# Optimization experiments

Measured on AMD Instinct MI355X. Metric: run time of the kernel, lower is better.

The kernel has to match this reference:

```python
import jax, jax.numpy as jnp
import numpy as np

COMMITMENT_COST = 0.25


def setup_inputs() -> dict:
    key = jax.random.key(0)
    k1, k2 = jax.random.split(key)
    x = jax.random.normal(k1, (32, 64, 64, 64), dtype=jnp.float32)  # NCHW, C=embedding_dim
    # nn.Embedding weight init: uniform(-1/num_embeddings, 1/num_embeddings)
    codebook = jax.random.uniform(k2, (512, 64), dtype=jnp.float32,
                                  minval=-1.0 / 512.0, maxval=1.0 / 512.0)
    return {"x": x, "codebook": codebook}


def reference(x, codebook):
    # NCHW -> NHWC
    inputs = jnp.transpose(x, (0, 2, 3, 1))  # [B,H,W,D]
    B, H, W, D = inputs.shape
    flat = inputs.reshape(-1, D)  # [N,D]
    # Squared Euclidean distances (argmin identical to torch.cdist's sqrt'ed distances)
    d2 = (jnp.sum(flat * flat, axis=1, keepdims=True)
          - 2.0 * flat @ codebook.T
          + jnp.sum(codebook * codebook, axis=1)[None, :])  # [N,K]
    idx = jnp.argmin(d2, axis=1)  # [N]
    quantized = codebook[idx].reshape(B, H, W, D)
    e_latent_loss = jnp.mean((jax.lax.stop_gradient(quantized) - inputs) ** 2)
    q_latent_loss = jnp.mean((quantized - jax.lax.stop_gradient(inputs)) ** 2)
    c_loss = q_latent_loss + COMMITMENT_COST * e_latent_loss
    # Straight-through estimator
    quantized = inputs + jax.lax.stop_gradient(quantized - inputs)
    quantized = jnp.transpose(quantized, (0, 3, 1, 2))  # NHWC -> NCHW
    return c_loss, quantized
```

## Files before the change

### kernel.cpp

```cpp
#include <hip/hip_runtime.h>
#include <hip/hip_bf16.h>


typedef __attribute__((ext_vector_type(8))) __bf16 bf16x8;
typedef __attribute__((ext_vector_type(4))) float f32x4;

#define WS_CBF   0
#define WS_HN2   65536
#define WS_RED   67584

#define K_XA   0
#define K_HN   8192
#define K_IDX  17408
#define K_RED  17664
#define K_SZ   17680

__device__ __forceinline__ unsigned f2b1(float f) {
  unsigned u = __float_as_uint(f);
  return (u + 0x7FFFu + ((u >> 16) & 1)) >> 16;
}
__device__ __forceinline__ unsigned pack2(float lo, float hi) {
  return f2b1(lo) | (f2b1(hi) << 16);
}
#if defined(__has_builtin)
#  if __has_builtin(__builtin_amdgcn_perm)
#    define PACKTR(lo, hi) __builtin_amdgcn_perm(__float_as_uint(hi), \
                             __float_as_uint(lo), 0x07060302u)
#  endif
#endif
#ifndef PACKTR
#  define PACKTR(lo, hi) ((__float_as_uint(hi) & 0xFFFF0000u) | \
                          (__float_as_uint(lo) >> 16))
#endif
__device__ __forceinline__ int swz(int row) {
  return ((row & 7) ^ ((row >> 4) & 7)) << 4;
}

__global__ void vq_prep(const float* __restrict__ cb, char* __restrict__ ws) {
  const int n = blockIdx.x * 64 + threadIdx.x;
  const float4* cb4 = (const float4*)cb;
  float4 f[16];
  #pragma unroll
  for (int j = 0; j < 16; ++j) f[j] = cb4[(n << 4) + j];
  float s = 0.f;
  #pragma unroll
  for (int j = 0; j < 16; ++j)
    s += f[j].x * f[j].x + f[j].y * f[j].y + f[j].z * f[j].z + f[j].w * f[j].w;
  ((float*)(ws + WS_HN2))[n] = 1.0f - 0.5f * s;
  const int ct = n >> 4, col = n & 15;
  #pragma unroll
  for (int kk = 0; kk < 2; ++kk) {
    #pragma unroll
    for (int g = 0; g < 4; ++g) {
      float4 a = f[kk * 8 + g * 2], b = f[kk * 8 + g * 2 + 1];
      uint4 u = {pack2(a.x, a.y), pack2(a.z, a.w), pack2(b.x, b.y), pack2(b.z, b.w)};
      *(uint4*)(ws + WS_CBF + (((ct << 1) + kk) << 10) + (((g << 4) | col) << 4)) = u;
    }
  }
}

__global__ void __launch_bounds__(128, 4)
vq_main(const float* __restrict__ x, const float* __restrict__ cb,
        const char* __restrict__ wsr, float* __restrict__ out,
        float* __restrict__ wsw) {
  __shared__ __align__(16) char smem[K_SZ];
  char*  xaz  = smem + K_XA;
  float* hn2z = (float*)(smem + K_HN);
  int*   idxz = (int*)(smem + K_IDX);
  float* redz = (float*)(smem + K_RED);
  float* qld2 = (float*)smem;

  const int t    = threadIdx.x;
  const int bid  = blockIdx.x;
  const int bimg = bid >> 6;
  const int hw0  = (bid & 63) << 6;
  const float4*  xb4 = (const float4*)(x + (bimg << 18) + hw0);
  const float4*  cb4 = (const float4*)cb;
  const bf16x8*  cbb = (const bf16x8*)(wsr + WS_CBF);

  float xsq = 0.f;
  {
    const int p  = t >> 2;
    const int r0 = (t & 3) << 4;
    #pragma unroll
    for (int j = 0; j < 4; ++j) {
      float4 A0 = xb4[((2 * p) << 10) + (r0 >> 2) + j];
      float4 A1 = xb4[((2 * p + 1) << 10) + (r0 >> 2) + j];
      const float* a0 = (const float*)&A0;
      const float* a1 = (const float*)&A1;
      #pragma unroll
      for (int u = 0; u < 4; ++u) {
        xsq = fmaf(a0[u], a0[u], xsq);
        xsq = fmaf(a1[u], a1[u], xsq);
        int r = r0 + (j << 2) + u;
        *(unsigned*)(xaz + r * 128 + ((p << 2) ^ swz(r))) = PACKTR(a0[u], a1[u]);
      }
    }
  }
  #pragma unroll
  for (int i = 0; i < 4; ++i)
    hn2z[t + (i << 7)] = ((const float*)(wsr + WS_HN2))[t + (i << 7)];
  __syncthreads();

  const int lane = t & 63;
  const int wid  = t >> 6;
  const int lrow = lane & 15;
  const int lk2  = (lane >> 4) << 4;

  bf16x8 af[2][2];
  #pragma unroll
  for (int s = 0; s < 2; ++s) {
    int row = (wid << 5) + (s << 4) + lrow;
    int sw = swz(row);
    af[s][0] = *(const bf16x8*)(xaz + row * 128 + (lk2 ^ sw));
    af[s][1] = *(const bf16x8*)(xaz + row * 128 + ((lk2 ^ 64) ^ sw));
  }

  unsigned bestu[2][4];
  #pragma unroll
  for (int s = 0; s < 2; ++s)
    #pragma unroll
    for (int r = 0; r < 4; ++r) bestu[s][r] = 0u;

  const unsigned tag0 = 511u - (unsigned)lrow;

  #pragma unroll 2
  for (int ct = 0; ct < 32; ++ct) {
    const bf16x8 b0 = cbb[(ct << 7) + lane];
    const bf16x8 b1 = cbb[(ct << 7) + 64 + lane];
    const float hv = hn2z[(ct << 4) + lrow];
    const unsigned tag = tag0 - (unsigned)(ct << 4);
    #pragma unroll
    for (int s = 0; s < 2; ++s) {
      f32x4 acc = {hv, hv, hv, hv};
      acc = __builtin_amdgcn_mfma_f32_16x16x32_bf16(af[s][0], b0, acc, 0, 0, 0);
      acc = __builtin_amdgcn_mfma_f32_16x16x32_bf16(af[s][1], b1, acc, 0, 0, 0);
      #pragma unroll
      for (int r = 0; r < 4; ++r) {
        unsigned key = (__float_as_uint(acc[r]) & 0xFFFFFE00u) | tag;
        bestu[s][r] = max(bestu[s][r], key);
      }
    }
  }

  float vsum = 0.f;
  #pragma unroll
  for (int s = 0; s < 2; ++s) {
    #pragma unroll
    for (int r = 0; r < 4; ++r) {
      unsigned k = bestu[s][r];
      #pragma unroll
      for (int m = 1; m <= 8; m <<= 1) {
        unsigned pk = __shfl_xor(k, m, 64);
        k = max(k, pk);
      }
      if (lrow == 0) {
        idxz[(wid << 5) + (s << 4) + ((lane >> 4) << 2) + r] =
            (int)(511u - (k & 511u));
        vsum += __uint_as_float(k & 0xFFFFFE00u) - 1.0f;
      }
    }
  }
  float lacc = xsq - 2.0f * vsum;
  #pragma unroll
  for (int m = 32; m; m >>= 1) lacc += __shfl_xor(lacc, m, 64);
  if (lane == 0) redz[wid] = lacc;
  __syncthreads();
  if (t == 0) wsw[bid] = redz[0] + redz[1];

  {
    const int myrow = t >> 1;
    const int chh   = t & 1;
    const int myidx = idxz[myrow];
    const float4* cbr = cb4 + (myidx << 4) + (chh << 3);
    #pragma unroll
    for (int j = 0; j < 8; ++j) {
      float4 v = cbr[j];
      const int d = (chh << 5) + (j << 2);
      qld2[(d + 0) * 68 + myrow] = v.x;
      qld2[(d + 1) * 68 + myrow] = v.y;
      qld2[(d + 2) * 68 + myrow] = v.z;
      qld2[(d + 3) * 68 + myrow] = v.w;
    }
  }
  __syncthreads();
  {
    float* outq = out + 1 + (bimg << 18) + hw0;
    const int r4 = (t & 15) << 2;
    const int d0 = t >> 4;
    #pragma unroll
    for (int i = 0; i < 8; ++i) {
      const int d = d0 + (i << 3);
      float4 v = *(const float4*)(qld2 + d * 68 + r4);
      *(float4*)(outq + (d << 12) + r4) = v;
    }
  }
}

__global__ void vq_finalize(const float* __restrict__ ws, float* __restrict__ out) {
  int t = threadIdx.x;
  __shared__ float red[4];
  float v = 0.f;
  #pragma unroll
  for (int k = 0; k < 8; ++k) v += ws[t + (k << 8)];
  #pragma unroll
  for (int m = 32; m; m >>= 1) v += __shfl_xor(v, m, 64);
  if ((t & 63) == 0) red[t >> 6] = v;
  __syncthreads();
  if (t == 0) out[0] = (red[0] + red[1] + red[2] + red[3]) * (1.25f / 8388608.0f);
}

extern "C" void kernel_launch(void* const* d_in, const int* in_sizes, int n_in,
                              void* d_out, int out_size, void* d_ws, size_t ws_size,
                              hipStream_t stream) {
  const float* x  = (const float*)d_in[0];
  const float* cb = (const float*)d_in[1];
  float* out = (float*)d_out;
  char*  ws  = (char*)d_ws;
  vq_prep<<<8, 64, 0, stream>>>(cb, ws);
  vq_main<<<2048, 128, 0, stream>>>(x, cb, ws, out, (float*)(ws + WS_RED));
  vq_finalize<<<1, 256, 0, stream>>>((float*)(ws + WS_RED), out);
}
```

Baseline: 33.94 us.

## Make each wavefront independent with private LDS regions and drop block barriers

Each of the two waves in a block now loads, transposes and gathers its own 32 rows in a private LDS region, which removes all three __syncthreads. The codebook-norm table is read straight from global (L1/L2-cached) memory instead of being staged into LDS. Per-wave partial losses are written out, so finalize sums twice as many entries. Nontemporal loads and stores are used for the streaming x input and the quantized output. The global norm reads inside the hot loop may add latency in exchange for less LDS traffic and no barriers.

```diff
diff --git a/kernel.cpp b/kernel.cpp
--- a/kernel.cpp
+++ b/kernel.cpp
@@ -9,11 +9,9 @@
 #define WS_HN2   65536
 #define WS_RED   67584
 
-#define K_XA   0
-#define K_HN   8192
-#define K_IDX  17408
-#define K_RED  17664
-#define K_SZ   17680
+#define WREG   9216
+#define K_IDX  18432
+#define K_SZ   18688
 
 __device__ __forceinline__ unsigned f2b1(float f) {
   unsigned u = __float_as_uint(f);
@@ -64,28 +62,30 @@
         const char* __restrict__ wsr, float* __restrict__ out,
         float* __restrict__ wsw) {
   __shared__ __align__(16) char smem[K_SZ];
-  char*  xaz  = smem + K_XA;
-  float* hn2z = (float*)(smem + K_HN);
-  int*   idxz = (int*)(smem + K_IDX);
-  float* redz = (float*)(smem + K_RED);
-  float* qld2 = (float*)smem;
-
   const int t    = threadIdx.x;
+  const int lane = t & 63;
+  const int wid  = t >> 6;
   const int bid  = blockIdx.x;
   const int bimg = bid >> 6;
-  const int hw0  = (bid & 63) << 6;
-  const float4*  xb4 = (const float4*)(x + (bimg << 18) + hw0);
-  const float4*  cb4 = (const float4*)cb;
-  const bf16x8*  cbb = (const bf16x8*)(wsr + WS_CBF);
+  const int wrow0 = ((bid & 63) << 6) + (wid << 5);
+
+  char*  xw   = smem + wid * WREG;
+  float* ovl  = (float*)(smem + wid * WREG);
+  int*   idxw = (int*)(smem + K_IDX) + (wid << 5);
+
+  const f32x4*  xb4  = (const f32x4*)(x + (bimg << 18) + wrow0);
+  const float4* cb4  = (const float4*)cb;
+  const bf16x8* cbb  = (const bf16x8*)(wsr + WS_CBF);
+  const float*  hn2g = (const float*)(wsr + WS_HN2);
 
   float xsq = 0.f;
   {
-    const int p  = t >> 2;
-    const int r0 = (t & 3) << 4;
+    const int p  = lane >> 1;
+    const int r0 = (lane & 1) << 4;
     #pragma unroll
     for (int j = 0; j < 4; ++j) {
-      float4 A0 = xb4[((2 * p) << 10) + (r0 >> 2) + j];
-      float4 A1 = xb4[((2 * p + 1) << 10) + (r0 >> 2) + j];
+      f32x4 A0 = __builtin_nontemporal_load(&xb4[((2 * p) << 10) + (r0 >> 2) + j]);
+      f32x4 A1 = __builtin_nontemporal_load(&xb4[((2 * p + 1) << 10) + (r0 >> 2) + j]);
       const float* a0 = (const float*)&A0;
       const float* a1 = (const float*)&A1;
       #pragma unroll
@@ -93,27 +93,21 @@
         xsq = fmaf(a0[u], a0[u], xsq);
         xsq = fmaf(a1[u], a1[u], xsq);
         int r = r0 + (j << 2) + u;
-        *(unsigned*)(xaz + r * 128 + ((p << 2) ^ swz(r))) = PACKTR(a0[u], a1[u]);
+        *(unsigned*)(xw + r * 128 + ((p << 2) ^ swz(r))) = PACKTR(a0[u], a1[u]);
       }
     }
   }
-  #pragma unroll
-  for (int i = 0; i < 4; ++i)
-    hn2z[t + (i << 7)] = ((const float*)(wsr + WS_HN2))[t + (i << 7)];
-  __syncthreads();
-
-  const int lane = t & 63;
-  const int wid  = t >> 6;
+
   const int lrow = lane & 15;
   const int lk2  = (lane >> 4) << 4;
 
   bf16x8 af[2][2];
   #pragma unroll
   for (int s = 0; s < 2; ++s) {
-    int row = (wid << 5) + (s << 4) + lrow;
+    int row = (s << 4) + lrow;
     int sw = swz(row);
-    af[s][0] = *(const bf16x8*)(xaz + row * 128 + (lk2 ^ sw));
-    af[s][1] = *(const bf16x8*)(xaz + row * 128 + ((lk2 ^ 64) ^ sw));
+    af[s][0] = *(const bf16x8*)(xw + row * 128 + (lk2 ^ sw));
+    af[s][1] = *(const bf16x8*)(xw + row * 128 + ((lk2 ^ 64) ^ sw));
   }
 
   unsigned bestu[2][4];
@@ -128,7 +122,7 @@
   for (int ct = 0; ct < 32; ++ct) {
     const bf16x8 b0 = cbb[(ct << 7) + lane];
     const bf16x8 b1 = cbb[(ct << 7) + 64 + lane];
-    const float hv = hn2z[(ct << 4) + lrow];
+    const float hv = hn2g[(ct << 4) + lrow];
     const unsigned tag = tag0 - (unsigned)(ct << 4);
     #pragma unroll
     for (int s = 0; s < 2; ++s) {
@@ -150,13 +144,9 @@
     for (int r = 0; r < 4; ++r) {
       unsigned k = bestu[s][r];
       #pragma unroll
-      for (int m = 1; m <= 8; m <<= 1) {
-        unsigned pk = __shfl_xor(k, m, 64);
-        k = max(k, pk);
-      }
+      for (int m = 1; m <= 8; m <<= 1) k = max(k, (unsigned)__shfl_xor(k, m, 64));
       if (lrow == 0) {
-        idxz[(wid << 5) + (s << 4) + ((lane >> 4) << 2) + r] =
-            (int)(511u - (k & 511u));
+        idxw[(s << 4) + ((lane >> 4) << 2) + r] = (int)(511u - (k & 511u));
         vsum += __uint_as_float(k & 0xFFFFFE00u) - 1.0f;
       }
     }
@@ -164,35 +154,32 @@
   float lacc = xsq - 2.0f * vsum;
   #pragma unroll
   for (int m = 32; m; m >>= 1) lacc += __shfl_xor(lacc, m, 64);
-  if (lane == 0) redz[wid] = lacc;
-  __syncthreads();
-  if (t == 0) wsw[bid] = redz[0] + redz[1];
+  if (lane == 0) wsw[(bid << 1) + wid] = lacc;
 
   {
-    const int myrow = t >> 1;
-    const int chh   = t & 1;
-    const int myidx = idxz[myrow];
-    const float4* cbr = cb4 + (myidx << 4) + (chh << 3);
+    const int row  = lane >> 1;
+    const int half = lane & 1;
+    const int myidx = idxw[row];
+    const float4* cbr = cb4 + (myidx << 4) + (half << 3);
     #pragma unroll
     for (int j = 0; j < 8; ++j) {
       float4 v = cbr[j];
-      const int d = (chh << 5) + (j << 2);
-      qld2[(d + 0) * 68 + myrow] = v.x;
-      qld2[(d + 1) * 68 + myrow] = v.y;
-      qld2[(d + 2) * 68 + myrow] = v.z;
-      qld2[(d + 3) * 68 + myrow] = v.w;
-    }
-  }
-  __syncthreads();
+      const int d = (half << 5) + (j << 2);
+      ovl[(d + 0) * 36 + row] = v.x;
+      ovl[(d + 1) * 36 + row] = v.y;
+      ovl[(d + 2) * 36 + row] = v.z;
+      ovl[(d + 3) * 36 + row] = v.w;
+    }
+  }
   {
-    float* outq = out + 1 + (bimg << 18) + hw0;
-    const int r4 = (t & 15) << 2;
-    const int d0 = t >> 4;
+    float* outq = out + 1 + (bimg << 18) + wrow0;
+    const int r4 = (lane & 7) << 2;
+    const int d0 = lane >> 3;
     #pragma unroll
     for (int i = 0; i < 8; ++i) {
       const int d = d0 + (i << 3);
-      float4 v = *(const float4*)(qld2 + d * 68 + r4);
-      *(float4*)(outq + (d << 12) + r4) = v;
+      f32x4 v = *(const f32x4*)(ovl + d * 36 + r4);
+      __builtin_nontemporal_store(v, (f32x4*)(outq + (d << 12) + r4));
     }
   }
 }
@@ -202,7 +189,7 @@
   __shared__ float red[4];
   float v = 0.f;
   #pragma unroll
-  for (int k = 0; k < 8; ++k) v += ws[t + (k << 8)];
+  for (int k = 0; k < 16; ++k) v += ws[t + (k << 8)];
   #pragma unroll
   for (int m = 32; m; m >>= 1) v += __shfl_xor(v, m, 64);
   if ((t & 63) == 0) red[t >> 6] = v;
```

Measured after the change: 45.80 us. 1.35x slower.

## Gather quantized output from transposed codebook, drop LDS staging and barriers

Applied to the files above, without the earlier changes.

The prep kernel now also writes a transposed fp32 codebook [D][K] to workspace. The main kernel broadcasts the argmin indices with shuffles and gathers the output directly from that transposed copy with float4 stores, so it no longer stages the result through LDS. That removes the index/transpose shared buffers and two __syncthreads. Per-wave loss partials go straight to workspace, and the finalize kernel sums twice as many entries. In exchange the output gathers become scattered scalar global loads, which should mostly hit in L2 since the transposed codebook is 128KB.

```diff
diff --git a/kernel.cpp b/kernel.cpp
--- a/kernel.cpp
+++ b/kernel.cpp
@@ -8,12 +8,11 @@
 #define WS_CBF   0
 #define WS_HN2   65536
 #define WS_RED   67584
+#define WS_CBT   83968
 
 #define K_XA   0
 #define K_HN   8192
-#define K_IDX  17408
-#define K_RED  17664
-#define K_SZ   17680
+#define K_SZ   10240
 
 __device__ __forceinline__ unsigned f2b1(float f) {
   unsigned u = __float_as_uint(f);
@@ -57,6 +56,15 @@
       *(uint4*)(ws + WS_CBF + (((ct << 1) + kk) << 10) + (((g << 4) | col) << 4)) = u;
     }
   }
+  float* cbt = (float*)(ws + WS_CBT);
+  #pragma unroll
+  for (int j = 0; j < 16; ++j) {
+    const int d0 = j << 2;
+    cbt[(d0 + 0) * 512 + n] = f[j].x;
+    cbt[(d0 + 1) * 512 + n] = f[j].y;
+    cbt[(d0 + 2) * 512 + n] = f[j].z;
+    cbt[(d0 + 3) * 512 + n] = f[j].w;
+  }
 }
 
 __global__ void __launch_bounds__(128, 4)
@@ -66,17 +74,14 @@
   __shared__ __align__(16) char smem[K_SZ];
   char*  xaz  = smem + K_XA;
   float* hn2z = (float*)(smem + K_HN);
-  int*   idxz = (int*)(smem + K_IDX);
-  float* redz = (float*)(smem + K_RED);
-  float* qld2 = (float*)smem;
 
   const int t    = threadIdx.x;
   const int bid  = blockIdx.x;
   const int bimg = bid >> 6;
   const int hw0  = (bid & 63) << 6;
-  const float4*  xb4 = (const float4*)(x + (bimg << 18) + hw0);
-  const float4*  cb4 = (const float4*)cb;
-  const bf16x8*  cbb = (const bf16x8*)(wsr + WS_CBF);
+  const float4* xb4 = (const float4*)(x + (bimg << 18) + hw0);
+  const bf16x8* cbb = (const bf16x8*)(wsr + WS_CBF);
+  const float*  cbt = (const float*)(wsr + WS_CBT);
 
   float xsq = 0.f;
   {
@@ -143,56 +148,53 @@
     }
   }
 
-  float vsum = 0.f;
   #pragma unroll
   for (int s = 0; s < 2; ++s) {
     #pragma unroll
     for (int r = 0; r < 4; ++r) {
       unsigned k = bestu[s][r];
       #pragma unroll
-      for (int m = 1; m <= 8; m <<= 1) {
-        unsigned pk = __shfl_xor(k, m, 64);
-        k = max(k, pk);
-      }
-      if (lrow == 0) {
-        idxz[(wid << 5) + (s << 4) + ((lane >> 4) << 2) + r] =
-            (int)(511u - (k & 511u));
-        vsum += __uint_as_float(k & 0xFFFFFE00u) - 1.0f;
-      }
-    }
-  }
-  float lacc = xsq - 2.0f * vsum;
-  #pragma unroll
-  for (int m = 32; m; m >>= 1) lacc += __shfl_xor(lacc, m, 64);
-  if (lane == 0) redz[wid] = lacc;
-  __syncthreads();
-  if (t == 0) wsw[bid] = redz[0] + redz[1];
+      for (int m = 1; m <= 8; m <<= 1) k = max(k, (unsigned)__shfl_xor(k, m, 64));
+      bestu[s][r] = k;
+    }
+  }
 
   {
-    const int myrow = t >> 1;
-    const int chh   = t & 1;
-    const int myidx = idxz[myrow];
-    const float4* cbr = cb4 + (myidx << 4) + (chh << 3);
+    float vsum = 0.f;
+    if (lrow == 0) {
+      #pragma unroll
+      for (int s = 0; s < 2; ++s)
+        #pragma unroll
+        for (int r = 0; r < 4; ++r)
+          vsum += __uint_as_float(bestu[s][r] & 0xFFFFFE00u) - 1.0f;
+    }
+    float lacc = xsq - 2.0f * vsum;
+    #pragma unroll
+    for (int m = 32; m; m >>= 1) lacc += __shfl_xor(lacc, m, 64);
+    if (lane == 0) wsw[(bid << 1) + wid] = lacc;
+  }
+
+  {
+    const int g  = lane & 7;
+    const int q  = g & 3;
+    const bool hi = (g & 4) != 0;
+    unsigned k0 = hi ? bestu[1][0] : bestu[0][0];
+    unsigned k1 = hi ? bestu[1][1] : bestu[0][1];
+    unsigned k2 = hi ? bestu[1][2] : bestu[0][2];
+    unsigned k3 = hi ? bestu[1][3] : bestu[0][3];
+    const int srcl = q << 4;
+    const int i0 = (int)(511u - ((unsigned)__shfl((int)k0, srcl, 64) & 511u));
+    const int i1 = (int)(511u - ((unsigned)__shfl((int)k1, srcl, 64) & 511u));
+    const int i2 = (int)(511u - ((unsigned)__shfl((int)k2, srcl, 64) & 511u));
+    const int i3 = (int)(511u - ((unsigned)__shfl((int)k3, srcl, 64) & 511u));
+    float* outq = out + 1 + (bimg << 18) + hw0 + (wid << 5) + (g << 2);
+    const int db = lane >> 3;
     #pragma unroll
     for (int j = 0; j < 8; ++j) {
-      float4 v = cbr[j];
-      const int d = (chh << 5) + (j << 2);
-      qld2[(d + 0) * 68 + myrow] = v.x;
-      qld2[(d + 1) * 68 + myrow] = v.y;
-      qld2[(d + 2) * 68 + myrow] = v.z;
-      qld2[(d + 3) * 68 + myrow] = v.w;
-    }
-  }
-  __syncthreads();
-  {
-    float* outq = out + 1 + (bimg << 18) + hw0;
-    const int r4 = (t & 15) << 2;
-    const int d0 = t >> 4;
-    #pragma unroll
-    for (int i = 0; i < 8; ++i) {
-      const int d = d0 + (i << 3);
-      float4 v = *(const float4*)(qld2 + d * 68 + r4);
-      *(float4*)(outq + (d << 12) + r4) = v;
+      const int d = db + (j << 3);
+      const float* base = cbt + (d << 9);
+      float4 v = {base[i0], base[i1], base[i2], base[i3]};
+      *(float4*)(outq + (d << 12)) = v;
     }
   }
 }
@@ -202,7 +204,7 @@
   __shared__ float red[4];
   float v = 0.f;
   #pragma unroll
-  for (int k = 0; k < 8; ++k) v += ws[t + (k << 8)];
+  for (int k = 0; k < 16; ++k) v += ws[t + (k << 8)];
   #pragma unroll
   for (int m = 32; m; m >>= 1) v += __shfl_xor(v, m, 64);
   if ((t & 63) == 0) red[t >> 6] = v;
```

After: 43.95 us. 1.29x slower.
